# Optimization experiments

Measured on AMD Instinct MI355X. Metric: run time of the kernel, lower is better.

The kernel has to match this reference:

```python
import jax, jax.numpy as jnp
import numpy as np

PH = PW = 7          # pooled output size
SR = 2               # sampling_ratio: SR x SR samples per bin
SCALES = (0.25, 0.125, 0.0625, 0.03125)  # FPN strides 4,8,16,32
K = 512              # number of ROIs
B = 2                # batch (images)
IMG = 800.0


def _coords(start, bsize, P):
    # sample coords for P bins, SR samples per bin: start + p*bin + (i+0.5)*bin/SR
    j = jnp.arange(P * SR, dtype=start.dtype)
    return (start[:, None]
            + (j // SR)[None, :] * bsize[:, None]
            + ((j % SR) + 0.5)[None, :] * (bsize[:, None] / SR))  # [K, P*SR]


def _roi_align_level(feat, rois, scale):
    # feat: [B, C, H, W] ; rois: [K, 5] (batch_idx, x1, y1, x2, y2 in image coords)
    Bf, C, H, W = feat.shape
    b = rois[:, 0].astype(jnp.int32)
    x1 = rois[:, 1] * scale
    y1 = rois[:, 2] * scale
    x2 = rois[:, 3] * scale
    y2 = rois[:, 4] * scale
    roi_w = jnp.maximum(x2 - x1, 1.0)   # legacy (aligned=False) ROIAlign
    roi_h = jnp.maximum(y2 - y1, 1.0)
    ys = _coords(y1, roi_h / PH, PH)    # [K, Sy]
    xs = _coords(x1, roi_w / PW, PW)    # [K, Sx]
    y = ys[:, :, None]                  # [K, Sy, 1]
    x = xs[:, None, :]                  # [K, 1, Sx]
    valid = (y > -1.0) & (y < H) & (x > -1.0) & (x < W)  # [K, Sy, Sx]
    yc = jnp.clip(y, 0.0, None)
    xc = jnp.clip(x, 0.0, None)
    yl = jnp.minimum(yc.astype(jnp.int32), H - 1)
    xl = jnp.minimum(xc.astype(jnp.int32), W - 1)
    yh = jnp.minimum(yl + 1, H - 1)
    xh = jnp.minimum(xl + 1, W - 1)
    ly = jnp.where(yl >= H - 1, 0.0, yc - yl)
    lx = jnp.where(xl >= W - 1, 0.0, xc - xl)
    hy, hx = 1.0 - ly, 1.0 - lx
    feat_flat = feat.reshape(Bf, C, H * W)
    Sy, Sx = PH * SR, PW * SR
    acc = jnp.zeros((rois.shape[0], C, Sy, Sx), feat.dtype)
    corners = ((yl, xl, hy * hx), (yl, xh, hy * lx),
               (yh, xl, ly * hx), (yh, xh, ly * lx))
    for yy, xx, w in corners:  # fixed 4-corner loop (not a data-dim loop)
        idx = jnp.broadcast_to(yy * W + xx, (rois.shape[0], Sy, Sx))
        vals = jax.vmap(lambda bi, ii: jnp.take(feat_flat, bi, axis=0)[:, ii])(b, idx)
        acc = acc + vals * jnp.broadcast_to(w, idx.shape)[:, None, :, :]
    acc = jnp.where(valid[:, None, :, :], acc, 0.0)
    # average SRxSR samples within each 7x7 bin
    return acc.reshape(rois.shape[0], C, PH, SR, PW, SR).mean(axis=(3, 5))


def setup_inputs() -> dict:
    key = jax.random.key(0)
    ks = jax.random.split(key, 10)
    input_0 = jax.random.normal(ks[0], (B, 256, 200, 200), jnp.float32)
    input_1 = jax.random.normal(ks[1], (B, 256, 100, 100), jnp.float32)
    input_2 = jax.random.normal(ks[2], (B, 256, 50, 50), jnp.float32)
    input_3 = jax.random.normal(ks[3], (B, 256, 25, 25), jnp.float32)
    bidx = jax.random.randint(ks[4], (K,), 0, B).astype(jnp.float32)
    x1 = jax.random.uniform(ks[5], (K,)) * (IMG - 64.0)
    y1 = jax.random.uniform(ks[6], (K,)) * (IMG - 64.0)
    bw = 32.0 + jax.random.uniform(ks[7], (K,)) * 200.0
    bh = 32.0 + jax.random.uniform(ks[8], (K,)) * 200.0
    rois = jnp.stack([bidx, x1, y1,
                      jnp.minimum(x1 + bw, IMG),
                      jnp.minimum(y1 + bh, IMG)], axis=1).astype(jnp.float32)
    level = jax.random.randint(ks[9], (K,), 0, 4).astype(jnp.int32)
    rois_counts = jnp.array([K // 2, K - K // 2], jnp.int32)  # unused (all ROIs valid)
    return {"input_0": input_0, "input_1": input_1, "input_2": input_2,
            "input_3": input_3, "rois": rois, "rois_counts": rois_counts,
            "level": level}


def reference(input_0, input_1, input_2, input_3, rois, rois_counts, level):
    feats = (input_0, input_1, input_2, input_3)
    lvl = level.astype(jnp.int32)
    out = jnp.zeros((rois.shape[0], input_0.shape[1], PH, PW), input_0.dtype)
    for i, (f, s) in enumerate(zip(feats, SCALES)):
        o = _roi_align_level(f, rois, s)
        out = out + jnp.where((lvl == i)[:, None, None, None], o, 0.0)
    return out
```

## Files before the change

kernel.cpp:

```cpp
#include <hip/hip_runtime.h>


#define NUM_CH 256

typedef float floatx2 __attribute__((ext_vector_type(2)));

__global__ __launch_bounds__(256) void roi_align_kernel(
    const float* __restrict__ f0,
    const float* __restrict__ f1,
    const float* __restrict__ f2,
    const float* __restrict__ f3,
    const float* __restrict__ rois_f,
    const int* __restrict__ level,
    float* __restrict__ out,
    int total)
{
    int b = blockIdx.x;
    int nb = gridDim.x;
    int wb = b;
    if ((nb & 7) == 0) {
        int per = nb >> 3;
        wb = (b & 7) * per + (b >> 3);
    }

    int e = wb * 256 + threadIdx.x;
    if (e >= total) return;

    int p  = e % 49;
    int t  = e / 49;
    int cp = t % (NUM_CH / 2);
    int k  = t / (NUM_CH / 2);
    int ph = p / 7;
    int pw = p % 7;
    int c0 = cp * 2;

    int lvl = level[k];
    const float* f;
    int H, W; float scale;
    if (lvl == 0)      { f = f0; H = 200; W = 200; scale = 0.25f;    }
    else if (lvl == 1) { f = f1; H = 100; W = 100; scale = 0.125f;   }
    else if (lvl == 2) { f = f2; H = 50;  W = 50;  scale = 0.0625f;  }
    else               { f = f3; H = 25;  W = 25;  scale = 0.03125f; }

    const float* rf = rois_f + (size_t)k * 5;
    float r0 = rf[0];
    float x1 = rf[1] * scale, y1 = rf[2] * scale;
    float x2 = rf[3] * scale, y2 = rf[4] * scale;
    int bi = (int)r0;
    bi = (bi < 0) ? 0 : ((bi > 1) ? 1 : bi);

    float bh = fmaxf(y2 - y1, 1.0f) * (1.0f / 7.0f);
    float bw = fmaxf(x2 - x1, 1.0f) * (1.0f / 7.0f);

    const size_t HW = (size_t)(H * W);
    const float* base0 = f + ((size_t)bi * NUM_CH + c0) * HW;

    int   rA[2], rB[2];
    float lyv[2], hyv[2], vy[2];
    #pragma unroll
    for (int sy = 0; sy < 2; ++sy) {
        float y = y1 + (float)ph * bh + ((float)sy + 0.5f) * (bh * 0.5f);
        bool valid = (y > -1.0f) && (y < (float)H);
        float yc = fmaxf(y, 0.0f);
        int yl = min((int)yc, H - 1);
        int yh = min(yl + 1, H - 1);
        float ly = (yl >= H - 1) ? 0.0f : (yc - (float)yl);
        rA[sy] = yl * W;
        rB[sy] = yh * W;
        lyv[sy] = ly; hyv[sy] = 1.0f - ly;
        vy[sy] = valid ? 0.25f : 0.0f;
    }
    int   xb[2];
    float lxv[2], hxv[2], sel[2], vx[2];
    #pragma unroll
    for (int sx = 0; sx < 2; ++sx) {
        float x = x1 + (float)pw * bw + ((float)sx + 0.5f) * (bw * 0.5f);
        bool valid = (x > -1.0f) && (x < (float)W);
        float xc = fmaxf(x, 0.0f);
        int xl = min((int)xc, W - 1);
        float lx = (xl >= W - 1) ? 0.0f : (xc - (float)xl);
        int xq = min(xl, W - 2);
        xb[sx] = xq;
        sel[sx] = (xl > xq) ? 1.0f : 0.0f;
        lxv[sx] = lx; hxv[sx] = 1.0f - lx;
        vx[sx] = valid ? 1.0f : 0.0f;
    }

    floatx2 va0[4], vb0[4], va1[4], vb1[4];
    #pragma unroll
    for (int s = 0; s < 4; ++s) {
        int sy = s >> 1, sx = s & 1;
        int oA = rA[sy] + xb[sx];
        int oB = rB[sy] + xb[sx];
        va0[s] = *(const floatx2*)(base0 + oA);
        vb0[s] = *(const floatx2*)(base0 + oB);
        va1[s] = *(const floatx2*)(base0 + HW + oA);
        vb1[s] = *(const floatx2*)(base0 + HW + oB);
    }

    float acc0 = 0.0f, acc1 = 0.0f;
    #pragma unroll
    for (int s = 0; s < 4; ++s) {
        int sy = s >> 1, sx = s & 1;
        float vs  = vy[sy] * vx[sx];
        float w00 = hyv[sy] * hxv[sx] * vs;
        float w01 = hyv[sy] * lxv[sx] * vs;
        float w10 = lyv[sy] * hxv[sx] * vs;
        float w11 = lyv[sy] * lxv[sx] * vs;
        float s0  = sel[sx];

        float a00 = va0[s].x + s0 * (va0[s].y - va0[s].x);
        float a10 = vb0[s].x + s0 * (vb0[s].y - vb0[s].x);
        acc0 += w00 * a00 + w01 * va0[s].y + w10 * a10 + w11 * vb0[s].y;

        float b00 = va1[s].x + s0 * (va1[s].y - va1[s].x);
        float b10 = vb1[s].x + s0 * (vb1[s].y - vb1[s].x);
        acc1 += w00 * b00 + w01 * va1[s].y + w10 * b10 + w11 * vb1[s].y;
    }

    size_t ob = ((size_t)k * NUM_CH + c0) * 49 + p;
    out[ob]      = acc0;
    out[ob + 49] = acc1;
}

extern "C" void kernel_launch(void* const* d_in, const int* in_sizes, int n_in,
                              void* d_out, int out_size, void* d_ws, size_t ws_size,
                              hipStream_t stream) {
    const float* f0   = (const float*)d_in[0];
    const float* f1   = (const float*)d_in[1];
    const float* f2   = (const float*)d_in[2];
    const float* f3   = (const float*)d_in[3];
    const float* rois = (const float*)d_in[4];
    const int* level = (const int*)d_in[6];
    float* out = (float*)d_out;

    int total = out_size / 2;
    int threads = 256;
    int blocks = (total + threads - 1) / threads;
    roi_align_kernel<<<blocks, threads, 0, stream>>>(f0, f1, f2, f3, rois, level, out, total);
}
```

Before: 200.9 us.

## Use one channel per thread with a float4 row-load path for narrow bins

Each thread now computes a single channel instead of two, which doubles the thread count and removes the XCD block-swizzle remap. When the bin width is under about four pixels, both x samples fall inside one 4-wide window, so each sample row needs a single float4 load and lanes are chosen with selects, replacing two float2 loads per row. Wider bins keep the old float2 path. The price is more threads repeating the ROI setup math, extra select instructions, and the loss of the cache locality the swizzle was meant to provide.

After: 186.4 us. 1.08x faster.

```diff
diff --git a/kernel.cpp b/kernel.cpp
--- a/kernel.cpp
+++ b/kernel.cpp
@@ -4,6 +4,14 @@
 #define NUM_CH 256
 
 typedef float floatx2 __attribute__((ext_vector_type(2)));
+typedef float floatx4 __attribute__((ext_vector_type(4)));
+
+__device__ __forceinline__ float ext4(floatx4 v, int i) {
+    float r = (i == 1) ? v.y : v.x;
+    r = (i == 2) ? v.z : r;
+    r = (i == 3) ? v.w : r;
+    return r;
+}
 
 __global__ __launch_bounds__(256) void roi_align_kernel(
     const float* __restrict__ f0,
@@ -15,24 +23,15 @@
     float* __restrict__ out,
     int total)
 {
-    int b = blockIdx.x;
-    int nb = gridDim.x;
-    int wb = b;
-    if ((nb & 7) == 0) {
-        int per = nb >> 3;
-        wb = (b & 7) * per + (b >> 3);
-    }
-
-    int e = wb * 256 + threadIdx.x;
+    int e = blockIdx.x * blockDim.x + threadIdx.x;
     if (e >= total) return;
 
     int p  = e % 49;
     int t  = e / 49;
-    int cp = t % (NUM_CH / 2);
-    int k  = t / (NUM_CH / 2);
+    int c  = t % NUM_CH;
+    int k  = t / NUM_CH;
     int ph = p / 7;
     int pw = p % 7;
-    int c0 = cp * 2;
 
     int lvl = level[k];
     const float* f;
@@ -52,8 +51,7 @@
     float bh = fmaxf(y2 - y1, 1.0f) * (1.0f / 7.0f);
     float bw = fmaxf(x2 - x1, 1.0f) * (1.0f / 7.0f);
 
-    const size_t HW = (size_t)(H * W);
-    const float* base0 = f + ((size_t)bi * NUM_CH + c0) * HW;
+    const float* base = f + ((size_t)bi * NUM_CH + c) * (size_t)(H * W);
 
     int   rA[2], rB[2];
     float lyv[2], hyv[2], vy[2];
@@ -70,8 +68,8 @@
         lyv[sy] = ly; hyv[sy] = 1.0f - ly;
         vy[sy] = valid ? 0.25f : 0.0f;
     }
-    int   xb[2];
-    float lxv[2], hxv[2], sel[2], vx[2];
+    int   xlv[2], xhv[2];
+    float lxv[2], hxv[2], vx[2];
     #pragma unroll
     for (int sx = 0; sx < 2; ++sx) {
         float x = x1 + (float)pw * bw + ((float)sx + 0.5f) * (bw * 0.5f);
@@ -79,48 +77,75 @@
         float xc = fmaxf(x, 0.0f);
         int xl = min((int)xc, W - 1);
         float lx = (xl >= W - 1) ? 0.0f : (xc - (float)xl);
-        int xq = min(xl, W - 2);
-        xb[sx] = xq;
-        sel[sx] = (xl > xq) ? 1.0f : 0.0f;
+        xlv[sx] = xl;
+        xhv[sx] = min(xl + 1, W - 1);
         lxv[sx] = lx; hxv[sx] = 1.0f - lx;
         vx[sx] = valid ? 1.0f : 0.0f;
     }
 
-    floatx2 va0[4], vb0[4], va1[4], vb1[4];
-    #pragma unroll
-    for (int s = 0; s < 4; ++s) {
-        int sy = s >> 1, sx = s & 1;
-        int oA = rA[sy] + xb[sx];
-        int oB = rB[sy] + xb[sx];
-        va0[s] = *(const floatx2*)(base0 + oA);
-        vb0[s] = *(const floatx2*)(base0 + oB);
-        va1[s] = *(const floatx2*)(base0 + HW + oA);
-        vb1[s] = *(const floatx2*)(base0 + HW + oB);
+    float acc = 0.0f;
+
+    if (bw <= 3.98f) {
+        int xq = min(xlv[0], W - 4);
+        int i0l = min(max(xlv[0] - xq, 0), 3);
+        int i0h = min(max(xhv[0] - xq, 0), 3);
+        int i1l = min(max(xlv[1] - xq, 0), 3);
+        int i1h = min(max(xhv[1] - xq, 0), 3);
+
+        floatx4 LA0 = *(const floatx4*)(base + rA[0] + xq);
+        floatx4 LB0 = *(const floatx4*)(base + rB[0] + xq);
+        floatx4 LA1 = *(const floatx4*)(base + rA[1] + xq);
+        floatx4 LB1 = *(const floatx4*)(base + rB[1] + xq);
+
+        #pragma unroll
+        for (int sy = 0; sy < 2; ++sy) {
+            floatx4 LA = sy ? LA1 : LA0;
+            floatx4 LB = sy ? LB1 : LB0;
+            #pragma unroll
+            for (int sx = 0; sx < 2; ++sx) {
+                int il = sx ? i1l : i0l;
+                int ih = sx ? i1h : i0h;
+                float vs  = vy[sy] * vx[sx];
+                float w00 = hyv[sy] * hxv[sx] * vs;
+                float w01 = hyv[sy] * lxv[sx] * vs;
+                float w10 = lyv[sy] * hxv[sx] * vs;
+                float w11 = lyv[sy] * lxv[sx] * vs;
+                acc += w00 * ext4(LA, il) + w01 * ext4(LA, ih)
+                     + w10 * ext4(LB, il) + w11 * ext4(LB, ih);
+            }
+        }
+    } else {
+        int   xb[2];
+        float sel[2];
+        #pragma unroll
+        for (int sx = 0; sx < 2; ++sx) {
+            int xq = min(xlv[sx], W - 2);
+            xb[sx]  = xq;
+            sel[sx] = (xlv[sx] > xq) ? 1.0f : 0.0f;
+        }
+        floatx2 va[4], vb[4];
+        #pragma unroll
+        for (int s = 0; s < 4; ++s) {
+            int sy = s >> 1, sx = s & 1;
+            va[s] = *(const floatx2*)(base + rA[sy] + xb[sx]);
+            vb[s] = *(const floatx2*)(base + rB[sy] + xb[sx]);
+        }
+        #pragma unroll
+        for (int s = 0; s < 4; ++s) {
+            int sy = s >> 1, sx = s & 1;
+            float vs  = vy[sy] * vx[sx];
+            float w00 = hyv[sy] * hxv[sx] * vs;
+            float w01 = hyv[sy] * lxv[sx] * vs;
+            float w10 = lyv[sy] * hxv[sx] * vs;
+            float w11 = lyv[sy] * lxv[sx] * vs;
+            float s0  = sel[sx];
+            float v00 = va[s].x + s0 * (va[s].y - va[s].x);
+            float v10 = vb[s].x + s0 * (vb[s].y - vb[s].x);
+            acc += w00 * v00 + w01 * va[s].y + w10 * v10 + w11 * vb[s].y;
+        }
     }
 
-    float acc0 = 0.0f, acc1 = 0.0f;
-    #pragma unroll
-    for (int s = 0; s < 4; ++s) {
-        int sy = s >> 1, sx = s & 1;
-        float vs  = vy[sy] * vx[sx];
-        float w00 = hyv[sy] * hxv[sx] * vs;
-        float w01 = hyv[sy] * lxv[sx] * vs;
-        float w10 = lyv[sy] * hxv[sx] * vs;
-        float w11 = lyv[sy] * lxv[sx] * vs;
-        float s0  = sel[sx];
-
-        float a00 = va0[s].x + s0 * (va0[s].y - va0[s].x);
-        float a10 = vb0[s].x + s0 * (vb0[s].y - vb0[s].x);
-        acc0 += w00 * a00 + w01 * va0[s].y + w10 * a10 + w11 * vb0[s].y;
-
-        float b00 = va1[s].x + s0 * (va1[s].y - va1[s].x);
-        float b10 = vb1[s].x + s0 * (vb1[s].y - vb1[s].x);
-        acc1 += w00 * b00 + w01 * va1[s].y + w10 * b10 + w11 * vb1[s].y;
-    }
-
-    size_t ob = ((size_t)k * NUM_CH + c0) * 49 + p;
-    out[ob]      = acc0;
-    out[ob + 49] = acc1;
+    out[e] = acc;
 }
 
 extern "C" void kernel_launch(void* const* d_in, const int* in_sizes, int n_in,
@@ -134,7 +159,7 @@
     const int* level = (const int*)d_in[6];
     float* out = (float*)d_out;
 
-    int total = out_size / 2;
+    int total = out_size;
     int threads = 256;
     int blocks = (total + threads - 1) / threads;
     roi_align_kernel<<<blocks, threads, 0, stream>>>(f0, f1, f2, f3, rois, level, out, total);
```
